# Kernel optimization log

Hardware: AMD Instinct MI355X
Metric: run time of the kernel (lower is better)

The kernel has to match this reference:

```python
import jax, jax.numpy as jnp
import numpy as np

EMBED_DIM = 1024
NUM_HEADS = 16
HEAD_DIM = EMBED_DIM // NUM_HEADS
SEQ_LEN = 2048
BATCH = 2


def setup_inputs() -> dict:
    key = jax.random.key(0)
    ks = jax.random.split(key, 9)
    s = 1.0 / np.sqrt(EMBED_DIM)
    inputs = jax.random.normal(ks[0], (BATCH, SEQ_LEN, EMBED_DIM), dtype=jnp.float32)
    Wq = jax.random.uniform(ks[1], (EMBED_DIM, EMBED_DIM), jnp.float32, -s, s)
    bq = jax.random.uniform(ks[2], (EMBED_DIM,), jnp.float32, -s, s)
    Wk = jax.random.uniform(ks[3], (EMBED_DIM, EMBED_DIM), jnp.float32, -s, s)
    bk = jax.random.uniform(ks[4], (EMBED_DIM,), jnp.float32, -s, s)
    Wv = jax.random.uniform(ks[5], (EMBED_DIM, EMBED_DIM), jnp.float32, -s, s)
    bv = jax.random.uniform(ks[6], (EMBED_DIM,), jnp.float32, -s, s)
    Wo = jax.random.uniform(ks[7], (EMBED_DIM, EMBED_DIM), jnp.float32, -s, s)
    bo = jax.random.uniform(ks[8], (EMBED_DIM,), jnp.float32, -s, s)
    return {"inputs": inputs, "Wq": Wq, "bq": bq, "Wk": Wk, "bk": bk,
            "Wv": Wv, "bv": bv, "Wo": Wo, "bo": bo}


def reference(inputs, Wq, bq, Wk, bk, Wv, bv, Wo, bo):
    B, S, D = inputs.shape
    H, Hd = NUM_HEADS, HEAD_DIM

    def heads(x):  # [B,S,D] -> [B,H,S,Hd]
        return x.reshape(B, S, H, Hd).transpose(0, 2, 1, 3)

    q = heads(inputs @ Wq + bq)
    k = heads(inputs @ Wk + bk)
    v = heads(inputs @ Wv + bv)

    # [B,H,S,S] causal scores (naive, matching original module)
    scores = jnp.einsum('bhqd,bhkd->bhqk', q, k) * (Hd ** -0.5)
    causal = jnp.tril(jnp.ones((S, S), dtype=bool))
    scores = jnp.where(causal, scores, jnp.float32(-jnp.inf))
    attn = jax.nn.softmax(scores, axis=-1)

    out = jnp.einsum('bhqk,bhkd->bhqd', attn, v)
    out = out.transpose(0, 2, 1, 3).reshape(B, S, D)
    return out @ Wo + bo
```

## Files before the change

### kernel.cpp

```cpp
#include <hip/hip_runtime.h>
#include <stdint.h>
#include <stddef.h>

#define SEQ   2048
#define DIM   1024
#define NH    16
#define HD    64
#define MTOT  4096
#define LPAD  72
#define EPAD  136
#define FPAD  132
#define QSCALE 0.18033688f

typedef __attribute__((ext_vector_type(8))) short short8;
typedef __attribute__((ext_vector_type(4))) float floatx4;
typedef __attribute__((ext_vector_type(16))) float floatx16;
typedef __attribute__((ext_vector_type(4))) float float4v;
typedef __attribute__((ext_vector_type(4))) unsigned short ushort4v;
typedef __attribute__((ext_vector_type(4))) unsigned int uint4v;

__device__ __forceinline__ floatx4 mfma_bf16(short8 a, short8 b, floatx4 c) {
    return __builtin_amdgcn_mfma_f32_16x16x32_bf16(a, b, c, 0, 0, 0);
}
__device__ __forceinline__ floatx16 mfma32(short8 a, short8 b, floatx16 c) {
    return __builtin_amdgcn_mfma_f32_32x32x16_bf16(a, b, c, 0, 0, 0);
}

__device__ __forceinline__ float b2f(unsigned short s) {
    unsigned int u = ((unsigned int)s) << 16;
    return __builtin_bit_cast(float, u);
}
__device__ __forceinline__ unsigned short f2b(float f) {
    unsigned int u = __builtin_bit_cast(unsigned int, f);
    u += 0x7fffu + ((u >> 16) & 1u);
    return (unsigned short)(u >> 16);
}
__device__ __forceinline__ unsigned int cvtpk(float lo, float hi) {
    unsigned int w;
    asm("v_cvt_pk_bf16_f32 %0, %1, %2" : "=v"(w) : "v"(lo), "v"(hi));
    return w;
}
__device__ __forceinline__ void swap32(unsigned int& a, unsigned int& b) {
    asm("v_permlane32_swap_b32 %0, %1" : "+v"(a), "+v"(b));
}
__device__ __forceinline__ float exp2v(float x) {
    float r;
    asm("v_exp_f32 %0, %1" : "=v"(r) : "v"(x));
    return r;
}
__device__ __forceinline__ short8 mk8(unsigned int a, unsigned int b,
                                      unsigned int c, unsigned int d) {
    uint4v u; u.x = a; u.y = b; u.z = c; u.w = d;
    return __builtin_bit_cast(short8, u);
}
__device__ __forceinline__ void g2l16(const unsigned short* g, unsigned short* l) {
    __builtin_amdgcn_global_load_lds(
        (const __attribute__((address_space(1))) void*)g,
        (__attribute__((address_space(3))) void*)l, 16, 0, 0);
}

__global__ __launch_bounds__(256) void prep_all(const float* __restrict__ w0,
                                                const float* __restrict__ w1,
                                                const float* __restrict__ w2,
                                                const float* __restrict__ w3,
                                                unsigned short* __restrict__ outbase,
                                                const float* __restrict__ xin,
                                                unsigned short* __restrict__ xout) {
    const int z = blockIdx.z;
    const int tid = threadIdx.x;
    if (z >= 4) {
        const int cblk = (z - 4) * 256 + blockIdx.y * 16 + blockIdx.x;
        const int i = (cblk * 256 + tid) * 4;
        const float4v v = *(const float4v*)&xin[i];
        ushort4v o;
        o.x = f2b(v.x); o.y = f2b(v.y); o.z = f2b(v.z); o.w = f2b(v.w);
        *(ushort4v*)&xout[i] = o;
        return;
    }
    __shared__ float t[64][65];
    const float* in = (z == 0) ? w0 : (z == 1) ? w1 : (z == 2) ? w2 : w3;
    unsigned short* out = outbase + (size_t)z * DIM * DIM;
    const int c0 = blockIdx.x * 64, r0 = blockIdx.y * 64;
    const int x = tid & 63, y = tid >> 6;
#pragma unroll
    for (int i = 0; i < 64; i += 4)
        t[y + i][x] = in[(size_t)(r0 + y + i) * DIM + c0 + x];
    __syncthreads();
#pragma unroll
    for (int i = 0; i < 64; i += 4)
        out[(size_t)(c0 + y + i) * DIM + r0 + x] = f2b(t[x][y + i]);
}

__global__ __launch_bounds__(256) void gemm_fused(const unsigned short* __restrict__ A,
                                                  const unsigned short* __restrict__ WTbase,
                                                  const float* __restrict__ b0,
                                                  const float* __restrict__ b1,
                                                  const float* __restrict__ b2,
                                                  void* __restrict__ outbase,
                                                  int qkv) {
    __shared__ __attribute__((aligned(16))) unsigned short smem[2 * 128 * LPAD];
    unsigned short* As = smem;
    unsigned short* Bs = smem + 128 * 64;

    const int z = blockIdx.z;
    const unsigned short* BT = WTbase + (size_t)z * (DIM * DIM);
    const float* bias        = (z == 0) ? b0 : (z == 1) ? b1 : b2;
    const int mode = qkv ? ((z == 0) ? 1 : (z == 1) ? 3 : 4) : 0;
    float* Cf          = (float*)outbase;
    unsigned short* Cb = (unsigned short*)outbase + (size_t)z * ((size_t)MTOT * DIM);

    const int tid = threadIdx.x;
    const int w = tid >> 6, lane = tid & 63;
    const int quad = lane >> 4, l16 = lane & 15;
    const int wm = w >> 1, wn = w & 1;
    const int m0 = blockIdx.x * 128, n0 = blockIdx.y * 128;
    const int bb = m0 >> 11;

    floatx4 acc[4][4];
#pragma unroll
    for (int mi = 0; mi < 4; ++mi)
#pragma unroll
        for (int ni = 0; ni < 4; ++ni) acc[mi][ni] = (floatx4)0.0f;

    const int srow8 = lane >> 3;
    const int sgs8  = ((lane & 7) ^ srow8) * 8;
    const unsigned short* gA = &A [(size_t)(m0 + w * 8 + srow8) * DIM + sgs8];
    const unsigned short* gB = &BT[(size_t)(n0 + w * 8 + srow8) * DIM + sgs8];

    const int sx = l16 & 7;

    for (int k0 = 0; ; k0 += 64) {
#pragma unroll
        for (int i = 0; i < 4; ++i) {
            g2l16(gA + (size_t)i * (32 * DIM) + k0, &As[(i * 4 + w) * 512]);
            g2l16(gB + (size_t)i * (32 * DIM) + k0, &Bs[(i * 4 + w) * 512]);
        }
        __syncthreads();
#pragma unroll
        for (int kk = 0; kk < 2; ++kk) {
            short8 a[4], b[4];
#pragma unroll
            for (int mi = 0; mi < 4; ++mi)
                a[mi] = *(const short8*)&As[(wm * 64 + mi * 16 + l16) * 64 +
                                            (((kk * 4) + quad) ^ sx) * 8];
#pragma unroll
            for (int ni = 0; ni < 4; ++ni)
                b[ni] = *(const short8*)&Bs[(wn * 64 + ni * 16 + l16) * 64 +
                                            (((kk * 4) + quad) ^ sx) * 8];
#pragma unroll
            for (int mi = 0; mi < 4; ++mi)
#pragma unroll
                for (int ni = 0; ni < 4; ++ni)
                    acc[mi][ni] = mfma_bf16(a[mi], b[ni], acc[mi][ni]);
        }
        if (k0 + 64 >= DIM) break;
        __syncthreads();
    }

    float bvv[4];
#pragma unroll
    for (int ni = 0; ni < 4; ++ni) bvv[ni] = bias[n0 + wn * 64 + ni * 16 + l16];

    if (mode == 0) {
        float* T = (float*)smem;
        for (int p = 0; p < 4; ++p) {
            __syncthreads();
            if (wm == (p >> 1)) {
                const int mib = (p & 1) * 2;
#pragma unroll
                for (int mm = 0; mm < 2; ++mm)
#pragma unroll
                    for (int ni = 0; ni < 4; ++ni)
#pragma unroll
                        for (int r = 0; r < 4; ++r)
                            T[(mm * 16 + quad * 4 + r) * FPAD + wn * 64 + ni * 16 + l16] =
                                acc[mib + mm][ni][r] + bvv[ni];
            }
            __syncthreads();
#pragma unroll
            for (int it = 0; it < 4; ++it) {
                const int c = it * 256 + tid;
                const int row = c >> 5, nof = (c & 31) * 4;
                *(float4v*)&Cf[(size_t)(m0 + p * 32 + row) * DIM + n0 + nof] =
                    *(const float4v*)&T[row * FPAD + nof];
            }
        }
    } else if (mode == 1) {
        unsigned short* T = smem;
        __syncthreads();
#pragma unroll
        for (int mi = 0; mi < 4; ++mi)
#pragma unroll
            for (int ni = 0; ni < 4; ++ni)
#pragma unroll
                for (int r = 0; r < 4; ++r)
                    T[(wm * 64 + mi * 16 + quad * 4 + r) * EPAD + wn * 64 + ni * 16 + l16] =
                        f2b((acc[mi][ni][r] + bvv[ni]) * QSCALE);
        __syncthreads();
#pragma unroll
        for (int it = 0; it < 8; ++it) {
            const int c = it * 256 + tid;
            const int seg = c >> 3, d8 = (c & 7) * 8;
            const int mm = seg >> 1, hseg = seg & 1;
            const int h = (n0 >> 6) + hseg;
            const int s = (m0 & (SEQ - 1)) + mm;
            *(short8*)&Cb[((size_t)(bb * NH + h) * SEQ + s) * HD + d8] =
                *(const short8*)&T[mm * EPAD + hseg * 64 + d8];
        }
    } else if (mode == 3) {
        unsigned short* T = smem;
        __syncthreads();
#pragma unroll
        for (int mi = 0; mi < 4; ++mi)
#pragma unroll
            for (int ni = 0; ni < 4; ++ni)
#pragma unroll
                for (int r = 0; r < 4; ++r)
                    T[(wm * 64 + mi * 16 + quad * 4 + r) * EPAD + wn * 64 + ni * 16 + l16] =
                        f2b(acc[mi][ni][r] + bvv[ni]);
        __syncthreads();
#pragma unroll
        for (int it = 0; it < 8; ++it) {
            const int f = it * 256 + tid;
            const int ln = f & 63, fragid = f >> 6;
            const int h2 = fragid >> 4;
            const int jb = (fragid >> 2) & 3;
            const int c  = fragid & 3;
            const short8 v = *(const short8*)&T[(jb * 32 + (ln & 31)) * EPAD +
                                                h2 * 64 + c * 16 + (ln >> 5) * 8];
            const int bh = bb * NH + (n0 >> 6) + h2;
            const int jg = ((m0 & (SEQ - 1)) >> 5) + jb;
            *(short8*)&Cb[(((size_t)bh * 64 + jg) * 4 + c) * 512 + ln * 8] = v;
        }
    } else {
        unsigned short* T = smem;
        __syncthreads();
#pragma unroll
        for (int mi = 0; mi < 4; ++mi)
#pragma unroll
            for (int ni = 0; ni < 4; ++ni) {
                ushort4v pk;
#pragma unroll
                for (int r = 0; r < 4; ++r) pk[r] = f2b(acc[mi][ni][r] + bvv[ni]);
                *(ushort4v*)&T[(wn * 64 + ni * 16 + l16) * EPAD + wm * 64 + mi * 16 + quad * 4] = pk;
            }
        __syncthreads();
#pragma unroll
        for (int it = 0; it < 8; ++it) {
            const int f = it * 256 + tid;
            const int ln = f & 63, fragid = f >> 6;
            const int h2 = fragid >> 4;
            const int jb = (fragid >> 2) & 3;
            const int dk = fragid & 3;
            const int d0 = dk >> 1, kk = dk & 1;
            const short8 v = *(const short8*)&T[(h2 * 64 + d0 * 32 + (ln & 31)) * EPAD +
                                                jb * 32 + kk * 16 + (ln >> 5) * 8];
            const int bh = bb * NH + (n0 >> 6) + h2;
            const int jg = ((m0 & (SEQ - 1)) >> 5) + jb;
            *(short8*)&Cb[(((size_t)bh * 64 + jg) * 4 + dk) * 512 + ln * 8] = v;
        }
    }
}

__global__ __launch_bounds__(64) void attn_fwd(const unsigned short* __restrict__ Q,
                                               const unsigned short* __restrict__ KP,
                                               const unsigned short* __restrict__ VP,
                                               unsigned short* __restrict__ O) {
    __shared__ __attribute__((aligned(16))) unsigned short Os[32 * LPAD];
    __shared__ float Linv[32];

    const int bh = blockIdx.x;
    const int qc = (gridDim.y - 1) - blockIdx.y;
    const int lane = threadIdx.x;
    const int ql  = lane & 31;
    const int hi  = lane >> 5;
    const int hi4 = hi * 4;
    const int hi8 = hi * 8;

    const unsigned short* Qh  = Q  + (size_t)bh * SEQ * HD;
    const unsigned short* KPh = KP + (size_t)bh * (64 * 2048);
    const unsigned short* VPh = VP + (size_t)bh * (64 * 2048);
    const int q0 = qc * 32;

    short8 qf[4];
#pragma unroll
    for (int c = 0; c < 4; ++c)
        qf[c] = *(const short8*)(Qh + (size_t)(q0 + ql) * HD + c * 16 + hi8);

    floatx16 o_acc0 = (floatx16)0.0f, o_acc1 = (floatx16)0.0f;
    float l0 = 0.0f, l1 = 0.0f;

    const unsigned short* kp = KPh + lane * 8;
    const unsigned short* vp = VPh + lane * 8;

#define LOADKV(KF, VF) do {                                                  \
        _Pragma("unroll")                                                    \
        for (int c_ = 0; c_ < 4; ++c_) {                                     \
            KF[c_] = *(const short8*)(kp + c_ * 512);                        \
            VF[c_] = *(const short8*)(vp + c_ * 512);                        \
        }                                                                    \
        kp += 2048; vp += 2048;                                              \
    } while (0)

#define ATT_BLOCK(KF, VF, MASKED) do {                                       \
        floatx16 st_ = (floatx16)0.0f;                                       \
        __builtin_amdgcn_s_setprio(1);                                       \
        _Pragma("unroll")                                                    \
        for (int c_ = 0; c_ < 4; ++c_) st_ = mfma32(KF[c_], qf[c_], st_);    \
        __builtin_amdgcn_s_setprio(0);                                       \
        float p_[16];                                                        \
        _Pragma("unroll")                                                    \
        for (int r_ = 0; r_ < 16; ++r_) {                                    \
            float e_ = exp2v(st_[r_]);                                       \
            if (MASKED)                                                      \
                e_ = (((r_ & 3) + 8 * (r_ >> 2) + hi4) > ql) ? 0.0f : e_;    \
            p_[r_] = e_;                                                     \
        }                                                                    \
        unsigned int w0_ = cvtpk(p_[0], p_[1]),   w2_ = cvtpk(p_[4], p_[5]); \
        unsigned int w1_ = cvtpk(p_[2], p_[3]),   w3_ = cvtpk(p_[6], p_[7]); \
        unsigned int w4_ = cvtpk(p_[8], p_[9]),   w6_ = cvtpk(p_[12], p_[13]); \
        unsigned int w5_ = cvtpk(p_[10], p_[11]), w7_ = cvtpk(p_[14], p_[15]); \
        swap32(w0_, w2_); swap32(w1_, w3_);                                  \
        swap32(w4_, w6_); swap32(w5_, w7_);                                  \
        const short8 pa0_ = mk8(w0_, w1_, w2_, w3_);                         \
        const short8 pa1_ = mk8(w4_, w5_, w6_, w7_);                         \
        __builtin_amdgcn_s_setprio(1);                                       \
        o_acc0 = mfma32(pa0_, VF[0], o_acc0);                                \
        o_acc1 = mfma32(pa0_, VF[2], o_acc1);                                \
        o_acc0 = mfma32(pa1_, VF[1], o_acc0);                                \
        o_acc1 = mfma32(pa1_, VF[3], o_acc1);                                \
        __builtin_amdgcn_s_setprio(0);                                       \
        l0 += (p_[0] + p_[1]) + (p_[2] + p_[3]);                             \
        l1 += (p_[4] + p_[5]) + (p_[6] + p_[7]);                             \
        l0 += (p_[8] + p_[9]) + (p_[10] + p_[11]);                           \
        l1 += (p_[12] + p_[13]) + (p_[14] + p_[15]);                         \
    } while (0)

    const int n = qc + 1;
    short8 kfA[4], vfA[4], kfB[4], vfB[4];
    LOADKV(kfA, vfA);
    int b = 0;
    while (b + 2 <= n - 1) {
        LOADKV(kfB, vfB);
        ATT_BLOCK(kfA, vfA, 0);
        LOADKV(kfA, vfA);
        ATT_BLOCK(kfB, vfB, 0);
        b += 2;
    }
    if (b == n - 2) {
        LOADKV(kfB, vfB);
        ATT_BLOCK(kfA, vfA, 0);
        ATT_BLOCK(kfB, vfB, 1);
    } else {
        ATT_BLOCK(kfA, vfA, 1);
    }

    float l = l0 + l1;
    l += __shfl_xor(l, 32, 64);
    const float inv = 1.0f / l;
    if (lane < 32) Linv[lane] = inv;
    __syncthreads();
#pragma unroll
    for (int r = 0; r < 16; ++r) {
        const int row = (r & 3) + 8 * (r >> 2) + hi4;
        const float iv = Linv[row];
        Os[row * LPAD + ql]      = f2b(o_acc0[r] * iv);
        Os[row * LPAD + 32 + ql] = f2b(o_acc1[r] * iv);
    }
    __syncthreads();
    const int bb = bh >> 4, h = bh & 15;
#pragma unroll
    for (int it = 0; it < 4; ++it) {
        const int row = it * 8 + (lane >> 3), d8 = (lane & 7) * 8;
        *(short8*)&O[(size_t)(bb * SEQ + q0 + row) * DIM + h * HD + d8] =
            *(const short8*)&Os[row * LPAD + d8];
    }
#undef LOADKV
#undef ATT_BLOCK
}

extern "C" void kernel_launch(void* const* d_in, const int* in_sizes, int n_in,
                              void* d_out, int out_size, void* d_ws, size_t ws_size,
                              hipStream_t stream) {
    const float* X  = (const float*)d_in[0];
    const float* Wq = (const float*)d_in[1];
    const float* bq = (const float*)d_in[2];
    const float* Wk = (const float*)d_in[3];
    const float* bk = (const float*)d_in[4];
    const float* Wv = (const float*)d_in[5];
    const float* bv = (const float*)d_in[6];
    const float* Wo = (const float*)d_in[7];
    const float* bo = (const float*)d_in[8];

    unsigned short* ws = (unsigned short*)d_ws;
    const size_t WSZ = (size_t)DIM * DIM;
    const size_t TSZ = (size_t)MTOT * DIM;
    unsigned short* WqT = ws;
    unsigned short* WoT = ws + 3 * WSZ;
    unsigned short* Qb  = ws + 4 * WSZ;
    unsigned short* Kp  = Qb + TSZ;
    unsigned short* Vp  = Kp + TSZ;
    unsigned short* Ob  = Vp + TSZ;

    unsigned short* Xb = (unsigned short*)d_out;

    prep_all<<<dim3(16, 16, 20), 256, 0, stream>>>(Wq, Wk, Wv, Wo, WqT, X, Xb);

    gemm_fused<<<dim3(MTOT / 128, DIM / 128, 3), 256, 0, stream>>>(
        Xb, WqT, bq, bk, bv, (void*)Qb, 1);

    attn_fwd<<<dim3(2 * NH, SEQ / 32), 64, 0, stream>>>(Qb, Kp, Vp, Ob);

    gemm_fused<<<dim3(MTOT / 128, DIM / 128, 1), 256, 0, stream>>>(
        Ob, WoT, bo, bo, bo, d_out, 0);
}
```

Baseline: 172.9 us.

## Software-pipeline attention loop: compute next block's QK before current softmax-PV

Splits the per-block attention step into a QK^T MFMA stage and a softmax+PV stage. The loop now issues the QK MFMAs for the next key block before doing exp/softmax and PV on the current one, so matrix-core work can overlap with the VALU exponentials. This keeps an extra 16-float score accumulator live, which raises register pressure and may lower occupancy.

```diff
diff --git a/kernel.cpp b/kernel.cpp
--- a/kernel.cpp
+++ b/kernel.cpp
@@ -302,16 +302,19 @@
         kp += 2048; vp += 2048;                                              \
     } while (0)
 
-#define ATT_BLOCK(KF, VF, MASKED) do {                                       \
-        floatx16 st_ = (floatx16)0.0f;                                       \
+#define QKB(ST, KF) do {                                                     \
+        ST = (floatx16)0.0f;                                                 \
         __builtin_amdgcn_s_setprio(1);                                       \
         _Pragma("unroll")                                                    \
-        for (int c_ = 0; c_ < 4; ++c_) st_ = mfma32(KF[c_], qf[c_], st_);    \
+        for (int c_ = 0; c_ < 4; ++c_) ST = mfma32(KF[c_], qf[c_], ST);      \
         __builtin_amdgcn_s_setprio(0);                                       \
+    } while (0)
+
+#define SMPV(ST, VF, MASKED) do {                                            \
         float p_[16];                                                        \
         _Pragma("unroll")                                                    \
         for (int r_ = 0; r_ < 16; ++r_) {                                    \
-            float e_ = exp2v(st_[r_]);                                       \
+            float e_ = exp2v(ST[r_]);                                        \
             if (MASKED)                                                      \
                 e_ = (((r_ & 3) + 8 * (r_ >> 2) + hi4) > ql) ? 0.0f : e_;    \
             p_[r_] = e_;                                                     \
@@ -338,21 +341,26 @@
 
     const int n = qc + 1;
     short8 kfA[4], vfA[4], kfB[4], vfB[4];
+    floatx16 stA, stB;
     LOADKV(kfA, vfA);
-    int b = 0;
-    while (b + 2 <= n - 1) {
+    QKB(stA, kfA);
+    int j = 1;
+    while (j + 1 < n) {
         LOADKV(kfB, vfB);
-        ATT_BLOCK(kfA, vfA, 0);
+        QKB(stB, kfB);
+        SMPV(stA, vfA, 0);
         LOADKV(kfA, vfA);
-        ATT_BLOCK(kfB, vfB, 0);
-        b += 2;
-    }
-    if (b == n - 2) {
+        QKB(stA, kfA);
+        SMPV(stB, vfB, 0);
+        j += 2;
+    }
+    if (j == n - 1) {
         LOADKV(kfB, vfB);
-        ATT_BLOCK(kfA, vfA, 0);
-        ATT_BLOCK(kfB, vfB, 1);
+        QKB(stB, kfB);
+        SMPV(stA, vfA, 0);
+        SMPV(stB, vfB, 1);
     } else {
-        ATT_BLOCK(kfA, vfA, 1);
+        SMPV(stA, vfA, 1);
     }
 
     float l = l0 + l1;
@@ -376,7 +384,8 @@
             *(const short8*)&Os[row * LPAD + d8];
     }
 #undef LOADKV
-#undef ATT_BLOCK
+#undef QKB
+#undef SMPV
 }
 
 extern "C" void kernel_launch(void* const* d_in, const int* in_sizes, int n_in,
```

New measurement: 170.5 us. Within noise of the previous version (-1.4%).

## Process 64-query tiles with two waves splitting KV blocks and merging partials

Applied to the files above, without the earlier changes.

The attention kernel now handles 64 query rows per block with two wavefronts. Each wave covers two 32-row query sub-tiles and alternate 32-key blocks, so every loaded K/V fragment is reused for two query tiles. The two waves' partial outputs and row sums are merged through fp32 shared memory before normalization. Query tiles are remapped in a zigzag order to balance causal work across the grid. The cost is more registers and LDS per block, half as many blocks, and an extra reduction step.

```diff
diff --git a/kernel.cpp b/kernel.cpp
--- a/kernel.cpp
+++ b/kernel.cpp
@@ -262,16 +262,19 @@
     }
 }
 
-__global__ __launch_bounds__(64) void attn_fwd(const unsigned short* __restrict__ Q,
-                                               const unsigned short* __restrict__ KP,
-                                               const unsigned short* __restrict__ VP,
-                                               unsigned short* __restrict__ O) {
-    __shared__ __attribute__((aligned(16))) unsigned short Os[32 * LPAD];
-    __shared__ float Linv[32];
+__global__ __launch_bounds__(128) void attn_fwd(const unsigned short* __restrict__ Q,
+                                                const unsigned short* __restrict__ KP,
+                                                const unsigned short* __restrict__ VP,
+                                                unsigned short* __restrict__ O) {
+    __shared__ float Fo[2][64][68];
+    __shared__ float Fl[2][64];
 
     const int bh = blockIdx.x;
-    const int qc = (gridDim.y - 1) - blockIdx.y;
-    const int lane = threadIdx.x;
+    const int y  = blockIdx.y;
+    const int g = y & 7, kq = y >> 3;
+    const int T = (kq == 0) ? g : (kq == 1) ? (15 - g) : (kq == 2) ? (16 + g) : (31 - g);
+    const int tid = threadIdx.x;
+    const int w = tid >> 6, lane = tid & 63;
     const int ql  = lane & 31;
     const int hi  = lane >> 5;
     const int hi4 = hi * 4;
@@ -280,18 +283,21 @@
     const unsigned short* Qh  = Q  + (size_t)bh * SEQ * HD;
     const unsigned short* KPh = KP + (size_t)bh * (64 * 2048);
     const unsigned short* VPh = VP + (size_t)bh * (64 * 2048);
-    const int q0 = qc * 32;
-
-    short8 qf[4];
-#pragma unroll
-    for (int c = 0; c < 4; ++c)
-        qf[c] = *(const short8*)(Qh + (size_t)(q0 + ql) * HD + c * 16 + hi8);
-
-    floatx16 o_acc0 = (floatx16)0.0f, o_acc1 = (floatx16)0.0f;
-    float l0 = 0.0f, l1 = 0.0f;
-
-    const unsigned short* kp = KPh + lane * 8;
-    const unsigned short* vp = VPh + lane * 8;
+    const int q0 = T * 64;
+
+    short8 qf0[4], qf1[4];
+#pragma unroll
+    for (int c = 0; c < 4; ++c) {
+        qf0[c] = *(const short8*)(Qh + (size_t)(q0 + ql) * HD + c * 16 + hi8);
+        qf1[c] = *(const short8*)(Qh + (size_t)(q0 + 32 + ql) * HD + c * 16 + hi8);
+    }
+
+    floatx16 o00 = (floatx16)0.0f, o01 = (floatx16)0.0f;
+    floatx16 o10 = (floatx16)0.0f, o11 = (floatx16)0.0f;
+    float lh0 = 0.0f, lh1 = 0.0f;
+
+    const unsigned short* kp = KPh + (size_t)w * 2048 + lane * 8;
+    const unsigned short* vp = VPh + (size_t)w * 2048 + lane * 8;
 
 #define LOADKV(KF, VF) do {                                                  \
         _Pragma("unroll")                                                    \
@@ -299,84 +305,131 @@
             KF[c_] = *(const short8*)(kp + c_ * 512);                        \
             VF[c_] = *(const short8*)(vp + c_ * 512);                        \
         }                                                                    \
-        kp += 2048; vp += 2048;                                              \
+        kp += 4096; vp += 4096;                 \
     } while (0)
 
-#define ATT_BLOCK(KF, VF, MASKED) do {                                       \
-        floatx16 st_ = (floatx16)0.0f;                                       \
+#define ATT2(KF, VF, M0, S0, M1) do {                                        \
+        floatx16 s0_ = (floatx16)0.0f, s1_ = (floatx16)0.0f;                 \
         __builtin_amdgcn_s_setprio(1);                                       \
         _Pragma("unroll")                                                    \
-        for (int c_ = 0; c_ < 4; ++c_) st_ = mfma32(KF[c_], qf[c_], st_);    \
+        for (int c_ = 0; c_ < 4; ++c_) s0_ = mfma32(KF[c_], qf0[c_], s0_);   \
+        _Pragma("unroll")                                                    \
+        for (int c_ = 0; c_ < 4; ++c_) s1_ = mfma32(KF[c_], qf1[c_], s1_);   \
         __builtin_amdgcn_s_setprio(0);                                       \
-        float p_[16];                                                        \
-        _Pragma("unroll")                                                    \
-        for (int r_ = 0; r_ < 16; ++r_) {                                    \
-            float e_ = exp2v(st_[r_]);                                       \
-            if (MASKED)                                                      \
-                e_ = (((r_ & 3) + 8 * (r_ >> 2) + hi4) > ql) ? 0.0f : e_;    \
-            p_[r_] = e_;                                                     \
+        if (!(S0)) {                                                         \
+            float p_[16];                                                    \
+            _Pragma("unroll")                                                \
+            for (int r_ = 0; r_ < 16; ++r_) {                                \
+                float e_ = exp2v(s0_[r_]);                                   \
+                if (M0)                                                      \
+                    e_ = (((r_ & 3) + 8 * (r_ >> 2) + hi4) > ql) ? 0.0f : e_; \
+                p_[r_] = e_;                                                 \
+            }                                                                \
+            unsigned int w0_ = cvtpk(p_[0], p_[1]),   w2_ = cvtpk(p_[4], p_[5]); \
+            unsigned int w1_ = cvtpk(p_[2], p_[3]),   w3_ = cvtpk(p_[6], p_[7]); \
+            unsigned int w4_ = cvtpk(p_[8], p_[9]),   w6_ = cvtpk(p_[12], p_[13]); \
+            unsigned int w5_ = cvtpk(p_[10], p_[11]), w7_ = cvtpk(p_[14], p_[15]); \
+            swap32(w0_, w2_); swap32(w1_, w3_);                              \
+            swap32(w4_, w6_); swap32(w5_, w7_);                              \
+            const short8 pa0_ = mk8(w0_, w1_, w2_, w3_);                     \
+            const short8 pa1_ = mk8(w4_, w5_, w6_, w7_);                     \
+            __builtin_amdgcn_s_setprio(1);                                   \
+            o00 = mfma32(pa0_, VF[0], o00);                                  \
+            o01 = mfma32(pa0_, VF[2], o01);                                  \
+            o00 = mfma32(pa1_, VF[1], o00);                                  \
+            o01 = mfma32(pa1_, VF[3], o01);                                  \
+            __builtin_amdgcn_s_setprio(0);                                   \
+            lh0 += ((p_[0] + p_[1]) + (p_[2] + p_[3]))                       \
+                 + ((p_[4] + p_[5]) + (p_[6] + p_[7]));                      \
+            lh0 += ((p_[8] + p_[9]) + (p_[10] + p_[11]))                     \
+                 + ((p_[12] + p_[13]) + (p_[14] + p_[15]));                  \
         }                                                                    \
-        unsigned int w0_ = cvtpk(p_[0], p_[1]),   w2_ = cvtpk(p_[4], p_[5]); \
-        unsigned int w1_ = cvtpk(p_[2], p_[3]),   w3_ = cvtpk(p_[6], p_[7]); \
-        unsigned int w4_ = cvtpk(p_[8], p_[9]),   w6_ = cvtpk(p_[12], p_[13]); \
-        unsigned int w5_ = cvtpk(p_[10], p_[11]), w7_ = cvtpk(p_[14], p_[15]); \
-        swap32(w0_, w2_); swap32(w1_, w3_);                                  \
-        swap32(w4_, w6_); swap32(w5_, w7_);                                  \
-        const short8 pa0_ = mk8(w0_, w1_, w2_, w3_);                         \
-        const short8 pa1_ = mk8(w4_, w5_, w6_, w7_);                         \
-        __builtin_amdgcn_s_setprio(1);                                       \
-        o_acc0 = mfma32(pa0_, VF[0], o_acc0);                                \
-        o_acc1 = mfma32(pa0_, VF[2], o_acc1);                                \
-        o_acc0 = mfma32(pa1_, VF[1], o_acc0);                                \
-        o_acc1 = mfma32(pa1_, VF[3], o_acc1);                                \
-        __builtin_amdgcn_s_setprio(0);                                       \
-        l0 += (p_[0] + p_[1]) + (p_[2] + p_[3]);                             \
-        l1 += (p_[4] + p_[5]) + (p_[6] + p_[7]);                             \
-        l0 += (p_[8] + p_[9]) + (p_[10] + p_[11]);                           \
-        l1 += (p_[12] + p_[13]) + (p_[14] + p_[15]);                         \
+        {                                                                    \
+            float p_[16];                                                    \
+            _Pragma("unroll")                                                \
+            for (int r_ = 0; r_ < 16; ++r_) {                                \
+                float e_ = exp2v(s1_[r_]);                                   \
+                if (M1)                                                      \
+                    e_ = (((r_ & 3) + 8 * (r_ >> 2) + hi4) > ql) ? 0.0f : e_; \
+                p_[r_] = e_;                                                 \
+            }                                                                \
+            unsigned int w0_ = cvtpk(p_[0], p_[1]),   w2_ = cvtpk(p_[4], p_[5]); \
+            unsigned int w1_ = cvtpk(p_[2], p_[3]),   w3_ = cvtpk(p_[6], p_[7]); \
+            unsigned int w4_ = cvtpk(p_[8], p_[9]),   w6_ = cvtpk(p_[12], p_[13]); \
+            unsigned int w5_ = cvtpk(p_[10], p_[11]), w7_ = cvtpk(p_[14], p_[15]); \
+            swap32(w0_, w2_); swap32(w1_, w3_);                              \
+            swap32(w4_, w6_); swap32(w5_, w7_);                              \
+            const short8 pa0_ = mk8(w0_, w1_, w2_, w3_);                     \
+            const short8 pa1_ = mk8(w4_, w5_, w6_, w7_);                     \
+            __builtin_amdgcn_s_setprio(1);                                   \
+            o10 = mfma32(pa0_, VF[0], o10);                                  \
+            o11 = mfma32(pa0_, VF[2], o11);                                  \
+            o10 = mfma32(pa1_, VF[1], o10);                                  \
+            o11 = mfma32(pa1_, VF[3], o11);                                  \
+            __builtin_amdgcn_s_setprio(0);                                   \
+            lh1 += ((p_[0] + p_[1]) + (p_[2] + p_[3]))                       \
+                 + ((p_[4] + p_[5]) + (p_[6] + p_[7]));                      \
+            lh1 += ((p_[8] + p_[9]) + (p_[10] + p_[11]))                     \
+                 + ((p_[12] + p_[13]) + (p_[14] + p_[15]));                  \
+        }                                                                    \
     } while (0)
 
-    const int n = qc + 1;
+    const int n = T + 1;
     short8 kfA[4], vfA[4], kfB[4], vfB[4];
     LOADKV(kfA, vfA);
     int b = 0;
     while (b + 2 <= n - 1) {
         LOADKV(kfB, vfB);
-        ATT_BLOCK(kfA, vfA, 0);
+        ATT2(kfA, vfA, 0, 0, 0);
         LOADKV(kfA, vfA);
-        ATT_BLOCK(kfB, vfB, 0);
+        ATT2(kfB, vfB, 0, 0, 0);
         b += 2;
     }
     if (b == n - 2) {
         LOADKV(kfB, vfB);
-        ATT_BLOCK(kfA, vfA, 0);
-        ATT_BLOCK(kfB, vfB, 1);
+        ATT2(kfA, vfA, 0, 0, 0);
+        if (w == 0) ATT2(kfB, vfB, 1, 0, 0);
+        else        ATT2(kfB, vfB, 0, 1, 1);
     } else {
-        ATT_BLOCK(kfA, vfA, 1);
-    }
-
-    float l = l0 + l1;
-    l += __shfl_xor(l, 32, 64);
-    const float inv = 1.0f / l;
-    if (lane < 32) Linv[lane] = inv;
-    __syncthreads();
+        if (w == 0) ATT2(kfA, vfA, 1, 0, 0);
+        else        ATT2(kfA, vfA, 0, 1, 1);
+    }
+
+    float* Fow = &Fo[w][0][0];
 #pragma unroll
     for (int r = 0; r < 16; ++r) {
         const int row = (r & 3) + 8 * (r >> 2) + hi4;
-        const float iv = Linv[row];
-        Os[row * LPAD + ql]      = f2b(o_acc0[r] * iv);
-        Os[row * LPAD + 32 + ql] = f2b(o_acc1[r] * iv);
-    }
+        Fow[row * 68 + ql]             = o00[r];
+        Fow[row * 68 + 32 + ql]        = o01[r];
+        Fow[(32 + row) * 68 + ql]      = o10[r];
+        Fow[(32 + row) * 68 + 32 + ql] = o11[r];
+    }
+    lh0 += __shfl_xor(lh0, 32, 64);
+    lh1 += __shfl_xor(lh1, 32, 64);
+    if (lane < 32) { Fl[w][lane] = lh0; Fl[w][32 + lane] = lh1; }
     __syncthreads();
+
     const int bb = bh >> 4, h = bh & 15;
 #pragma unroll
     for (int it = 0; it < 4; ++it) {
-        const int row = it * 8 + (lane >> 3), d8 = (lane & 7) * 8;
+        const int row = it * 16 + (tid >> 3);
+        const int d8  = (tid & 7) * 8;
+        const float* s0 = &Fo[0][row][d8];
+        const float* s1 = &Fo[1][row][d8];
+        const float4v a0 = *(const float4v*)&s0[0];
+        const float4v a1 = *(const float4v*)&s0[4];
+        const float4v b0 = *(const float4v*)&s1[0];
+        const float4v b1 = *(const float4v*)&s1[4];
+        const float iv = 1.0f / (Fl[0][row] + Fl[1][row]);
+        const unsigned int u0 = cvtpk((a0.x + b0.x) * iv, (a0.y + b0.y) * iv);
+        const unsigned int u1 = cvtpk((a0.z + b0.z) * iv, (a0.w + b0.w) * iv);
+        const unsigned int u2 = cvtpk((a1.x + b1.x) * iv, (a1.y + b1.y) * iv);
+        const unsigned int u3 = cvtpk((a1.z + b1.z) * iv, (a1.w + b1.w) * iv);
         *(short8*)&O[(size_t)(bb * SEQ + q0 + row) * DIM + h * HD + d8] =
-            *(const short8*)&Os[row * LPAD + d8];
+            mk8(u0, u1, u2, u3);
     }
 #undef LOADKV
-#undef ATT_BLOCK
+#undef ATT2
 }
 
 extern "C" void kernel_launch(void* const* d_in, const int* in_sizes, int n_in,
@@ -409,7 +462,7 @@
     gemm_fused<<<dim3(MTOT / 128, DIM / 128, 3), 256, 0, stream>>>(
         Xb, WqT, bq, bk, bv, (void*)Qb, 1);
 
-    attn_fwd<<<dim3(2 * NH, SEQ / 32), 64, 0, stream>>>(Qb, Kp, Vp, Ob);
+    attn_fwd<<<dim3(2 * NH, SEQ / 64), 128, 0, stream>>>(Qb, Kp, Vp, Ob);
 
     gemm_fused<<<dim3(MTOT / 128, DIM / 128, 1), 256, 0, stream>>>(
         Ob, WoT, bo, bo, bo, d_out, 0);
```

Measured after the change: 170.7 us. About the same (-1.3%).
